# Kernel optimization log

Hardware: AMD Instinct MI355X
Metric: run time of the kernel (lower is better)

## Reference

```python
import jax, jax.numpy as jnp
import numpy as np

M = 4096      # dictionary_size
D = 64        # feature dim
YD = 4        # output dim (y_dim)
FF = 0.999    # forgetting_factor
REG = 1e-2    # regularisation
JITTER = 1e-10
LS = 8.0      # RBF lengthscale


def rbf(a, b):
    # squared-distance RBF Gram via the ||a||^2 + ||b||^2 - 2ab^T identity
    a2 = jnp.sum(a * a, -1)[:, None]
    b2 = jnp.sum(b * b, -1)[None, :]
    d2 = jnp.maximum(a2 + b2 - 2.0 * (a @ b.T), 0.0)
    return jnp.exp(-d2 / (2.0 * LS * LS))


def setup_inputs() -> dict:
    key = jax.random.key(0)
    ks = jax.random.split(key, 7)
    return {
        'dictionary': jax.random.normal(ks[0], (M, D), jnp.float32),
        'mu': jax.random.normal(ks[1], (YD, M, 1), jnp.float32),
        'sigma': jax.random.normal(ks[2], (M, M), jnp.float32),
        'Q': jax.random.normal(ks[3], (M, M), jnp.float32),
        'x': jax.random.normal(ks[4], (D,), jnp.float32),
        'y': jax.random.normal(ks[5], (YD,), jnp.float32),
        'noise_num': jax.random.uniform(ks[6], (YD, 1, 1), jnp.float32),
        'noise_den': jnp.ones((1,), jnp.float32),
        'time_index': jnp.arange(M, dtype=jnp.float32),
        't': M,
    }


def reference(dictionary, mu, sigma, Q, x, y, noise_num, noise_den, time_index, t):
    alloc = time_index >= 0.0                      # (M,) bool: allocated slots
    y_ = y[:, None, None]                          # (YD,1,1)

    # --- B2P forgetting ---
    Kdd = rbf(dictionary, dictionary) * (alloc[:, None] * alloc[None, :])
    sig = FF * sigma + (1.0 - FF) * Kdd
    mu_f = jnp.sqrt(FF) * mu

    # --- kernel evals for new sample ---
    K_dx = rbf(dictionary, x[None, :]) * alloc[:, None]   # (M,1)
    K_xx = rbf(x[None, :], x[None, :]) + JITTER           # (1,1)

    q_ = Q @ K_dx                                         # (M,1)
    pu = jnp.maximum(K_xx - K_dx.T @ q_, 0.0)             # projection uncertainty (1,1)
    h_ = sig @ q_                                         # (M,1)
    npv = jnp.maximum(pu + q_.T @ h_, 0.0)                # noiseless predictive var (1,1)
    pred_mean = q_.T @ mu_f                               # (YD,1,1) via batched matmul
    pv = REG + npv

    # --- augmented (M+1) state ---
    p_ = jnp.concatenate((h_, npv), axis=-2)              # (M+1,1)
    mu_a = jnp.concatenate((mu_f, pred_mean), axis=-2) + (y_ - pred_mean) / pv * p_
    sig_a = jnp.block([[sig, h_], [h_.T, npv]]) - (p_ @ p_.T) / pv
    p2 = jnp.concatenate((q_, -jnp.ones((1, 1), q_.dtype)), axis=0)
    Q_a = jnp.pad(Q, ((0, 1), (0, 1))) + (p2 @ p2.T) / pu

    nnum = noise_num + FF * (y_ - pred_mean) ** 2 / pv
    nden = noise_den + FF

    # --- pruning criterion ---
    x_alloc = jnp.concatenate((alloc, jnp.ones((1,), bool)))

    def crit_low(_):
        return jnp.concatenate((jnp.ones((M, 1), Q_a.dtype), jnp.zeros((1, 1), Q_a.dtype)))

    def crit_mse(_):
        dq = jnp.where(~x_alloc, jnp.inf, jnp.diag(Q_a))
        errors = Q_a @ mu_a / dq[:, None]                 # (YD,M+1,1)
        return jnp.abs(errors).sum(-3)                    # (M+1,1)

    criterion = jax.lax.cond(pu.squeeze() < JITTER, crit_low, crit_mse, None)
    prune = jnp.argmin(criterion)
    denom = jnp.where(~x_alloc[prune], jnp.inf, Q_a[prune, prune])

    # swap (prune <-> last) permutation, then drop last row/col
    perm = jnp.arange(M + 1)
    perm = jnp.where(perm == prune, M, jnp.where(perm == M, prune, perm))

    Q_r = Q_a[perm, :]                                    # row swap
    Qs = Q_r[:-1, prune]                                  # column `prune` after row swap
    Q_n = Q_r[:, perm][:M, :M] - jnp.outer(Qs, Qs) / denom

    mu_n = mu_a[:, perm, :][:, :M, :]
    sig_n = sig_a[perm, :][:, perm][:M, :M]

    dict_n = dictionary.at[prune].set(x)
    ti_n = time_index.at[prune].set(jnp.asarray(t, time_index.dtype))
    alloc_n = ti_n >= 0.0
    sig_n = (alloc_n[:, None] * alloc_n[None, :]) * sig_n
    mu_n = jnp.where((ti_n < 0.0)[:, None], 0.0, mu_n)

    return (mu_n, sig_n, Q_n, dict_n, ti_n, nnum, nden)
```

## Files before the change

kernel.cpp:

```cpp
#include <hip/hip_runtime.h>
#include <math.h>

#define Mn 4096
#define Dn 64

#define OFF_A2   0
#define OFF_K    4096
#define OFF_Q    8192
#define OFF_H    12288
#define OFF_CRIT 20480
#define OFF_QS   32800
#define OFF_QSD  36896
#define SC_PU    40992
#define SC_INVPU 40993
#define SC_NPV   40994
#define SC_PV    40995
#define SC_INVPV 40996
#define SC_DENOM 40997
#define SC_PRUNE 40998
#define SC_DL    41000
#define SC_VY    41004
#define SC_MUAM  41008
#define OFF_DICTB 49152

#define O_MU   0
#define O_SIG  16384
#define O_Q    16793600
#define O_DICT 33570816
#define O_TI   33832960
#define O_NNUM 33837056
#define O_NDEN 33837060

typedef __attribute__((ext_vector_type(8))) __bf16 bf16x8;
typedef __attribute__((ext_vector_type(4))) float f32x4;

__device__ __forceinline__ float waveReduceSum(float v) {
#pragma unroll
    for (int o = 32; o > 0; o >>= 1) v += __shfl_down(v, o);
    return v;
}

__device__ __forceinline__ unsigned short f2bf_rne(float f) {
    unsigned u = __float_as_uint(f);
    unsigned r = (u + 0x7FFFu + ((u >> 16) & 1u)) >> 16;
    return (unsigned short)r;
}

__global__ void k1_prep(const float* __restrict__ dict, const float* __restrict__ x,
                        const float* __restrict__ ti, float* __restrict__ ws) {
    int row  = blockIdx.x * 4 + (threadIdx.x >> 6);
    int lane = threadIdx.x & 63;
    float d  = dict[row * Dn + lane];
    float xv = x[lane];
    ((unsigned short*)(ws + OFF_DICTB))[row * Dn + lane] = f2bf_rne(d);
    float a2 = waveReduceSum(d * d);
    float x2 = waveReduceSum(xv * xv);
    float dx = waveReduceSum(d * xv);
    if (lane == 0) {
        ws[OFF_A2 + row] = a2;
        float d2 = fmaxf(a2 + x2 - 2.0f * dx, 0.0f);
        float kv = expf(d2 * (-1.0f / 128.0f));
        ws[OFF_K + row] = (ti[row] >= 0.0f) ? kv : 0.0f;
    }
}

__global__ void k2_q(const float* __restrict__ Q, float* __restrict__ ws) {
    __shared__ float red[4];
    const int row = blockIdx.x;
    const int tid = threadIdx.x;
    const float4* Qr = (const float4*)(Q + (size_t)row * Mn);
    const float4* kv = (const float4*)(ws + OFF_K);
    float s = 0.0f;
#pragma unroll
    for (int it = 0; it < 4; ++it) {
        int u = tid + it * 256;
        float4 a = Qr[u], b = kv[u];
        s += a.x * b.x + a.y * b.y + a.z * b.z + a.w * b.w;
    }
    s = waveReduceSum(s);
    if ((tid & 63) == 0) red[tid >> 6] = s;
    __syncthreads();
    if (tid == 0) {
        ws[OFF_Q + row] = red[0] + red[1] + red[2] + red[3];
        ws[OFF_H + row] = 0.0f;
    }
}

__global__ __launch_bounds__(256) void k3_h(
        const float* __restrict__ sigma, const float* __restrict__ ti,
        float* __restrict__ ws) {
    const int tid  = threadIdx.x;
    const int lane = tid & 63;
    const int w    = tid >> 6;

    if (blockIdx.x < 1024) {
        const int row = blockIdx.x * 4 + w;
        const float4* S  = (const float4*)(sigma + (size_t)row * Mn);
        const float4* q4 = (const float4*)(ws + OFF_Q);
        float s = 0.0f;
#pragma unroll
        for (int it = 0; it < 16; ++it) {
            int u = lane + it * 64;
            float4 a = S[u], b = q4[u];
            s += a.x * b.x + a.y * b.y + a.z * b.z + a.w * b.w;
        }
        s = waveReduceSum(s);
        if (lane == 0) atomicAdd(ws + OFF_H + row, 0.999f * s);
        return;
    }

    const int t  = blockIdx.x - 1024;
    const int i0 = (t >> 5) * 128 + (w >> 1) * 64;
    const int j0 = (t & 31) * 128 + (w & 1) * 64;
    const int lr = lane >> 4;
    const int lc = lane & 15;
    const uint4* db = (const uint4*)(ws + OFF_DICTB);

    bf16x8 bfrag[4][2];
    float a2j[4], qmj[4];
#pragma unroll
    for (int jt = 0; jt < 4; ++jt) {
        const int col = j0 + jt * 16 + lc;
        bfrag[jt][0] = __builtin_bit_cast(bf16x8, db[col * 8 + lr]);
        bfrag[jt][1] = __builtin_bit_cast(bf16x8, db[col * 8 + 4 + lr]);
        a2j[jt] = ws[OFF_A2 + col];
        float alj = (ti[col] >= 0.0f) ? 1.0f : 0.0f;
        qmj[jt] = 0.001f * alj * ws[OFF_Q + col];
    }

#pragma unroll
    for (int it = 0; it < 4; ++it) {
        const int arow = i0 + it * 16 + lc;
        bf16x8 af0 = __builtin_bit_cast(bf16x8, db[arow * 8 + lr]);
        bf16x8 af1 = __builtin_bit_cast(bf16x8, db[arow * 8 + 4 + lr]);
        float hacc[4] = {0.f, 0.f, 0.f, 0.f};
        float a2i[4], ali[4];
#pragma unroll
        for (int i = 0; i < 4; ++i) {
            const int rg = i0 + it * 16 + lr * 4 + i;
            a2i[i] = ws[OFF_A2 + rg];
            ali[i] = (ti[rg] >= 0.0f) ? 1.0f : 0.0f;
        }
#pragma unroll
        for (int jt = 0; jt < 4; ++jt) {
            f32x4 acc = {0.0f, 0.0f, 0.0f, 0.0f};
            acc = __builtin_amdgcn_mfma_f32_16x16x32_bf16(af0, bfrag[jt][0], acc, 0, 0, 0);
            acc = __builtin_amdgcn_mfma_f32_16x16x32_bf16(af1, bfrag[jt][1], acc, 0, 0, 0);
#pragma unroll
            for (int i = 0; i < 4; ++i) {
                float d2 = fmaxf(a2i[i] + a2j[jt] - 2.0f * acc[i], 0.0f);
                float kv = __expf(d2 * (-1.0f / 128.0f)) * ali[i];
                hacc[i] = fmaf(kv, qmj[jt], hacc[i]);
            }
        }
#pragma unroll
        for (int i = 0; i < 4; ++i) {
            float v = hacc[i];
            v += __shfl_xor(v, 1);
            v += __shfl_xor(v, 2);
            v += __shfl_xor(v, 4);
            v += __shfl_xor(v, 8);
            if (lc == i) atomicAdd(ws + OFF_H + i0 + it * 16 + lr * 4 + i, v);
        }
    }
}

__device__ __forceinline__ float blockReduce1024(float v, float* sred) {
    v = waveReduceSum(v);
    int tid = threadIdx.x;
    __syncthreads();
    if ((tid & 63) == 0) sred[tid >> 6] = v;
    __syncthreads();
    float r = 0.0f;
    if (tid == 0) {
#pragma unroll
        for (int i = 0; i < 16; ++i) r += sred[i];
    }
    return r;
}

__global__ __launch_bounds__(1024) void k4_scalars(
        const float* __restrict__ mu, const float* __restrict__ y,
        const float* __restrict__ nn, const float* __restrict__ nd,
        float* __restrict__ ws, float* __restrict__ out) {
    __shared__ float sred[16];
    const int tid = threadIdx.x;
    const float* k = ws + OFF_K;
    const float* q = ws + OFF_Q;
    const float* h = ws + OFF_H;
    float kq = 0, qh = 0, p0 = 0, p1 = 0, p2 = 0, p3 = 0;
    for (int i = tid; i < Mn; i += 1024) {
        float qi = q[i];
        kq += k[i] * qi;
        qh += qi * h[i];
        p0 += qi * mu[0 * Mn + i];
        p1 += qi * mu[1 * Mn + i];
        p2 += qi * mu[2 * Mn + i];
        p3 += qi * mu[3 * Mn + i];
    }
    float rkq = blockReduce1024(kq, sred);
    float rqh = blockReduce1024(qh, sred);
    float r0 = blockReduce1024(p0, sred);
    float r1 = blockReduce1024(p1, sred);
    float r2 = blockReduce1024(p2, sred);
    float r3 = blockReduce1024(p3, sred);
    if (tid == 0) {
        const float sf = sqrtf(0.999f);
        float pu  = fmaxf(1.0f - rkq, 0.0f);
        float npv = fmaxf(pu + rqh, 0.0f);
        float pv  = 0.01f + npv;
        ws[SC_PU] = pu;
        ws[SC_INVPU] = 1.0f / pu;
        ws[SC_NPV] = npv;
        ws[SC_PV] = pv;
        ws[SC_INVPV] = 1.0f / pv;
        float rr[4] = {r0, r1, r2, r3};
        float critM = 0.0f;
#pragma unroll
        for (int yd = 0; yd < 4; ++yd) {
            float pm = sf * rr[yd];
            float dy = y[yd] - pm;
            float dl = dy / pv;
            float muaM = pm + dl * npv;
            float vy   = (sf * rr[yd] + dl * rqh) - muaM;
            ws[SC_DL + yd]   = dl;
            ws[SC_VY + yd]   = vy;
            ws[SC_MUAM + yd] = muaM;
            critM += fabsf(vy);
            out[O_NNUM + yd] = nn[yd] + 0.999f * (dy * dy) / pv;
        }
        out[O_NDEN] = nd[0] + 0.999f;
        ws[OFF_CRIT + Mn] = (pu < 1e-10f) ? 0.0f : critM;
    }
}

__global__ __launch_bounds__(256) void k5_crit(const float* __restrict__ Q,
                                               const float* __restrict__ mu,
                                               const float* __restrict__ ti,
                                               float* __restrict__ ws) {
    const int row  = blockIdx.x * 4 + (threadIdx.x >> 6);
    const int lane = threadIdx.x & 63;
    const float pu = ws[SC_PU];
    if (pu < 1e-10f) {
        if (lane == 0) ws[OFF_CRIT + row] = 1.0f;
        return;
    }
    const float4* Qr4 = (const float4*)(Q + (size_t)row * Mn);
    const float4* m04 = (const float4*)(mu + 0 * Mn);
    const float4* m14 = (const float4*)(mu + 1 * Mn);
    const float4* m24 = (const float4*)(mu + 2 * Mn);
    const float4* m34 = (const float4*)(mu + 3 * Mn);
    const float4* h4  = (const float4*)(ws + OFF_H);
    float am0 = 0, am1 = 0, am2 = 0, am3 = 0, ah = 0;
#pragma unroll
    for (int it = 0; it < 16; ++it) {
        int u = lane + it * 64;
        float4 qv = Qr4[u];
        float4 a0 = m04[u], a1 = m14[u], a2 = m24[u], a3 = m34[u], hh = h4[u];
        am0 += qv.x * a0.x + qv.y * a0.y + qv.z * a0.z + qv.w * a0.w;
        am1 += qv.x * a1.x + qv.y * a1.y + qv.z * a1.z + qv.w * a1.w;
        am2 += qv.x * a2.x + qv.y * a2.y + qv.z * a2.z + qv.w * a2.w;
        am3 += qv.x * a3.x + qv.y * a3.y + qv.z * a3.z + qv.w * a3.w;
        ah  += qv.x * hh.x + qv.y * hh.y + qv.z * hh.z + qv.w * hh.w;
    }
    am0 = waveReduceSum(am0);
    am1 = waveReduceSum(am1);
    am2 = waveReduceSum(am2);
    am3 = waveReduceSum(am3);
    ah  = waveReduceSum(ah);
    if (lane == 0) {
        const float inv_pu = ws[SC_INVPU];
        const float sf = sqrtf(0.999f);
        float qrow = ws[OFF_Q + row];
        float dq = Q[(size_t)row * Mn + row] + qrow * qrow * inv_pu;
        float crit = 0.0f;
        float am[4] = {am0, am1, am2, am3};
#pragma unroll
        for (int yd = 0; yd < 4; ++yd) {
            float e = sf * am[yd] + ws[SC_DL + yd] * ah + ws[SC_VY + yd] * inv_pu * qrow;
            crit += fabsf(e / dq);
        }
        bool xa = (ti[row] >= 0.0f);
        ws[OFF_CRIT + row] = xa ? crit : 0.0f;
    }
}

__global__ __launch_bounds__(1024) void k6_argmin(const float* __restrict__ Q,
                                                  const float* __restrict__ ti,
                                                  float* __restrict__ ws) {
    __shared__ float sval[1024];
    __shared__ int   sidx[1024];
    const int tid = threadIdx.x;
    float bv = INFINITY;
    int bi = Mn + 1;
    for (int i = tid; i <= Mn; i += 1024) {
        float v = ws[OFF_CRIT + i];
        if (v < bv) { bv = v; bi = i; }
    }
    sval[tid] = bv; sidx[tid] = bi;
    __syncthreads();
    for (int s = 512; s > 0; s >>= 1) {
        if (tid < s) {
            float ov = sval[tid + s]; int oi = sidx[tid + s];
            if (ov < sval[tid] || (ov == sval[tid] && oi < sidx[tid])) {
                sval[tid] = ov; sidx[tid] = oi;
            }
        }
        __syncthreads();
    }
    if (tid == 0) {
        int prune = sidx[0];
        ((int*)ws)[SC_PRUNE] = prune;
        float inv_pu = ws[SC_INVPU];
        bool xa = (prune == Mn) ? true : (ti[prune] >= 0.0f);
        float qap;
        if (prune < Mn) {
            float qp = ws[OFF_Q + prune];
            qap = Q[(size_t)prune * Mn + prune] + qp * qp * inv_pu;
        } else {
            qap = inv_pu;
        }
        ws[SC_DENOM] = xa ? qap : INFINITY;
    }
}

__global__ void k6b_vec(const float* __restrict__ Q, const float* __restrict__ dict,
                        const float* __restrict__ x, const float* __restrict__ ti,
                        const int* __restrict__ tptr, float* __restrict__ ws,
                        float* __restrict__ out) {
    const int tid = blockIdx.x * 256 + threadIdx.x;
    const int prune = ((const int*)ws)[SC_PRUNE];
    const int row = tid >> 6, col = tid & 63;
    out[O_DICT + tid] = (row == prune) ? x[col] : dict[tid];
    if (tid < Mn) {
        float tv = ti[tid];
        if (tid == prune) {
            int raw = *tptr;
            tv = (raw >= 0 && raw < (1 << 30)) ? (float)raw : __int_as_float(raw);
        }
        out[O_TI + tid] = tv;
        const float inv_pu = ws[SC_INVPU];
        const float denom  = ws[SC_DENOM];
        const float p2p = (prune < Mn) ? ws[OFF_Q + prune] : -1.0f;
        float qs;
        if (tid == prune) {
            qs = -p2p * inv_pu;
        } else {
            float base = (prune < Mn) ? Q[(size_t)tid * Mn + prune] : 0.0f;
            qs = base + ws[OFF_Q + tid] * p2p * inv_pu;
        }
        ws[OFF_QS + tid] = qs;
        ws[OFF_QSD + tid] = qs / denom;
    }
}

__global__ __launch_bounds__(256) void k7_fused(const float* __restrict__ Q,
                                                const float* __restrict__ sigma,
                                                const float* __restrict__ mu,
                                                const float* __restrict__ ti,
                                                float* __restrict__ out,
                                                const float* __restrict__ ws) {
    const int tid = threadIdx.x;
    const int prune = ((const int*)ws)[SC_PRUNE];
    const float inv_pu = ws[SC_INVPU];
    const float inv_pv = ws[SC_INVPV];
    const float npv = ws[SC_NPV];

    if (blockIdx.x >= 1024) {
        const int i = blockIdx.x - 1024;
        const int pi = (i == prune) ? Mn : i;
        const bool piok = (pi < Mn);
        const float p2i = piok ? ws[OFF_Q + pi] : -1.0f;
        const float qsi = ws[OFF_QS + i];
        const float4* Qr4  = (const float4*)(Q + (size_t)pi * Mn);
        const float4* q4   = (const float4*)(ws + OFF_Q);
        const float4* qsd4 = (const float4*)(ws + OFF_QSD);
        float4* o4 = (float4*)(out + O_Q + (size_t)i * Mn);
#pragma unroll
        for (int it = 0; it < 4; ++it) {
            int u = tid + it * 256;
            float4 base = piok ? Qr4[u] : make_float4(0.f, 0.f, 0.f, 0.f);
            float4 p2j = q4[u];
            if ((prune >> 2) == u) {
                int c = prune & 3;
                ((float*)&p2j)[c] = -1.0f;
                ((float*)&base)[c] = 0.0f;
            }
            float4 d = qsd4[u];
            float4 r;
            r.x = base.x + p2i * p2j.x * inv_pu - qsi * d.x;
            r.y = base.y + p2i * p2j.y * inv_pu - qsi * d.y;
            r.z = base.z + p2i * p2j.z * inv_pu - qsi * d.z;
            r.w = base.w + p2i * p2j.w * inv_pu - qsi * d.w;
            o4[u] = r;
        }
        if (tid < 4) {
            float tin = out[O_TI + i];
            float v;
            if (tin < 0.0f) v = 0.0f;
            else if (i == prune) v = ws[SC_MUAM + tid];
            else {
                const float sf = sqrtf(0.999f);
                v = sf * mu[tid * Mn + i] + ws[SC_DL + tid] * ws[OFF_H + i];
            }
            out[O_MU + tid * Mn + i] = v;
        }
        return;
    }

    const int t    = blockIdx.x;
    const int lane = tid & 63;
    const int w    = tid >> 6;
    const int i0 = (t >> 5) * 128 + (w >> 1) * 64;
    const int j0 = (t & 31) * 128 + (w & 1) * 64;
    const int lr = lane >> 4;
    const int lc = lane & 15;
    const uint4* db = (const uint4*)(ws + OFF_DICTB);

    bf16x8 bfI[4][2];
    float a2i_s[4], alio_s[4], ain_s[4], hr_s[4];
    bool prow_s[4];
#pragma unroll
    for (int it = 0; it < 4; ++it) {
        const int ri = i0 + it * 16 + lc;
        bfI[it][0] = __builtin_bit_cast(bf16x8, db[ri * 8 + lr]);
        bfI[it][1] = __builtin_bit_cast(bf16x8, db[ri * 8 + 4 + lr]);
        a2i_s[it]  = ws[OFF_A2 + ri];
        alio_s[it] = (ti[ri] >= 0.0f) ? 1.0f : 0.0f;
        ain_s[it]  = (out[O_TI + ri] >= 0.0f) ? 1.0f : 0.0f;
        hr_s[it]   = ws[OFF_H + ri];
        prow_s[it] = (ri == prune);
    }

#pragma unroll
    for (int jt = 0; jt < 4; ++jt) {
        const int jrow = j0 + jt * 16 + lc;
        bf16x8 afJ0 = __builtin_bit_cast(bf16x8, db[jrow * 8 + lr]);
        bf16x8 afJ1 = __builtin_bit_cast(bf16x8, db[jrow * 8 + 4 + lr]);
        const int cb = j0 + jt * 16 + lr * 4;
        const float4 a2j4 = *(const float4*)(ws + OFF_A2 + cb);
        const float4 hj4  = *(const float4*)(ws + OFF_H + cb);
        const float4 tio4 = *(const float4*)(ti + cb);
        const float4 tin4 = *(const float4*)(out + O_TI + cb);
        float a2j[4] = {a2j4.x, a2j4.y, a2j4.z, a2j4.w};
        float hj[4]  = {hj4.x, hj4.y, hj4.z, hj4.w};
        float aljo[4] = {tio4.x >= 0.f ? 1.f : 0.f, tio4.y >= 0.f ? 1.f : 0.f,
                         tio4.z >= 0.f ? 1.f : 0.f, tio4.w >= 0.f ? 1.f : 0.f};
        float ajn[4]  = {tin4.x >= 0.f ? 1.f : 0.f, tin4.y >= 0.f ? 1.f : 0.f,
                         tin4.z >= 0.f ? 1.f : 0.f, tin4.w >= 0.f ? 1.f : 0.f};
        bool pcol[4] = {cb + 0 == prune, cb + 1 == prune, cb + 2 == prune, cb + 3 == prune};
#pragma unroll
        for (int it = 0; it < 4; ++it) {
            f32x4 acc = {0.0f, 0.0f, 0.0f, 0.0f};
            acc = __builtin_amdgcn_mfma_f32_16x16x32_bf16(afJ0, bfI[it][0], acc, 0, 0, 0);
            acc = __builtin_amdgcn_mfma_f32_16x16x32_bf16(afJ1, bfI[it][1], acc, 0, 0, 0);
            const int rg = i0 + it * 16 + lc;
            const size_t off = (size_t)rg * Mn + cb;
            const float4 sv4 = *(const float4*)(sigma + off);
            float sv[4] = {sv4.x, sv4.y, sv4.z, sv4.w};
            float res[4];
#pragma unroll
            for (int e = 0; e < 4; ++e) {
                float d2 = fmaxf(a2i_s[it] + a2j[e] - 2.0f * acc[e], 0.0f);
                float kv = __expf(d2 * (-1.0f / 128.0f)) * alio_s[it] * aljo[e];
                float bs = 0.999f * sv[e] + 0.001f * kv;
                if (pcol[e])    bs = prow_s[it] ? npv : hr_s[it];
                if (prow_s[it]) bs = pcol[e] ? npv : hj[e];
                float p_i = prow_s[it] ? npv : hr_s[it];
                float p_j = pcol[e] ? npv : hj[e];
                res[e] = ain_s[it] * ajn[e] * (bs - p_i * p_j * inv_pv);
            }
            float4 r4 = {res[0], res[1], res[2], res[3]};
            *(float4*)(out + O_SIG + off) = r4;
        }
    }
}

extern "C" void kernel_launch(void* const* d_in, const int* in_sizes, int n_in,
                              void* d_out, int out_size, void* d_ws, size_t ws_size,
                              hipStream_t stream) {
    const float* dict  = (const float*)d_in[0];
    const float* mu    = (const float*)d_in[1];
    const float* sigma = (const float*)d_in[2];
    const float* Q     = (const float*)d_in[3];
    const float* x     = (const float*)d_in[4];
    const float* y     = (const float*)d_in[5];
    const float* nn    = (const float*)d_in[6];
    const float* nd    = (const float*)d_in[7];
    const float* ti    = (const float*)d_in[8];
    const int*   tptr  = (const int*)d_in[9];
    float* out = (float*)d_out;
    float* ws  = (float*)d_ws;

    k1_prep<<<1024, 256, 0, stream>>>(dict, x, ti, ws);
    k2_q<<<4096, 256, 0, stream>>>(Q, ws);
    k3_h<<<2048, 256, 0, stream>>>(sigma, ti, ws);
    k4_scalars<<<1, 1024, 0, stream>>>(mu, y, nn, nd, ws, out);
    k5_crit<<<1024, 256, 0, stream>>>(Q, mu, ti, ws);
    k6_argmin<<<1, 1024, 0, stream>>>(Q, ti, ws);
    k6b_vec<<<1024, 256, 0, stream>>>(Q, dict, x, ti, tptr, ws, out);
    k7_fused<<<5120, 256, 0, stream>>>(Q, sigma, mu, ti, out, ws);
}
```

Baseline: 337.1 us.

## Batch loads ahead of use, prefetch sigma tiles, and use nontemporal stores

Restructures the streaming dot-product kernels so that all global loads for a chunk are issued before the arithmetic, exposing more memory-level parallelism. The fused output kernel now software-prefetches the next sigma tile while computing the current one, and writes Q and sigma outputs with nontemporal stores to avoid polluting cache. It also adds an occupancy hint to the launch bounds. This raises register pressure, which could limit occupancy or cause spills.

```diff
diff --git a/kernel.cpp b/kernel.cpp
--- a/kernel.cpp
+++ b/kernel.cpp
@@ -46,6 +46,11 @@
     return (unsigned short)r;
 }
 
+__device__ __forceinline__ void nt_store4(float* p, float a, float b, float c, float d) {
+    f32x4 v = {a, b, c, d};
+    __builtin_nontemporal_store(v, (f32x4*)p);
+}
+
 __global__ void k1_prep(const float* __restrict__ dict, const float* __restrict__ x,
                         const float* __restrict__ ti, float* __restrict__ ws) {
     int row  = blockIdx.x * 4 + (threadIdx.x >> 6);
@@ -64,19 +69,22 @@
     }
 }
 
-__global__ void k2_q(const float* __restrict__ Q, float* __restrict__ ws) {
+__global__ __launch_bounds__(256, 4) void k2_q(const float* __restrict__ Q,
+                                               float* __restrict__ ws) {
     __shared__ float red[4];
     const int row = blockIdx.x;
     const int tid = threadIdx.x;
     const float4* Qr = (const float4*)(Q + (size_t)row * Mn);
     const float4* kv = (const float4*)(ws + OFF_K);
+    float4 a[4], b[4];
+#pragma unroll
+    for (int it = 0; it < 4; ++it) a[it] = Qr[tid + it * 256];
+#pragma unroll
+    for (int it = 0; it < 4; ++it) b[it] = kv[tid + it * 256];
     float s = 0.0f;
 #pragma unroll
-    for (int it = 0; it < 4; ++it) {
-        int u = tid + it * 256;
-        float4 a = Qr[u], b = kv[u];
-        s += a.x * b.x + a.y * b.y + a.z * b.z + a.w * b.w;
-    }
+    for (int it = 0; it < 4; ++it)
+        s += a[it].x * b[it].x + a[it].y * b[it].y + a[it].z * b[it].z + a[it].w * b[it].w;
     s = waveReduceSum(s);
     if ((tid & 63) == 0) red[tid >> 6] = s;
     __syncthreads();
@@ -86,7 +94,7 @@
     }
 }
 
-__global__ __launch_bounds__(256) void k3_h(
+__global__ __launch_bounds__(256, 4) void k3_h(
         const float* __restrict__ sigma, const float* __restrict__ ti,
         float* __restrict__ ws) {
     const int tid  = threadIdx.x;
@@ -99,10 +107,15 @@
         const float4* q4 = (const float4*)(ws + OFF_Q);
         float s = 0.0f;
 #pragma unroll
-        for (int it = 0; it < 16; ++it) {
-            int u = lane + it * 64;
-            float4 a = S[u], b = q4[u];
-            s += a.x * b.x + a.y * b.y + a.z * b.z + a.w * b.w;
+        for (int c = 0; c < 2; ++c) {
+            float4 a[8], b[8];
+#pragma unroll
+            for (int j = 0; j < 8; ++j) a[j] = S[lane + (c * 8 + j) * 64];
+#pragma unroll
+            for (int j = 0; j < 8; ++j) b[j] = q4[lane + (c * 8 + j) * 64];
+#pragma unroll
+            for (int j = 0; j < 8; ++j)
+                s += a[j].x * b[j].x + a[j].y * b[j].y + a[j].z * b[j].z + a[j].w * b[j].w;
         }
         s = waveReduceSum(s);
         if (lane == 0) atomicAdd(ws + OFF_H + row, 0.999f * s);
@@ -234,10 +247,10 @@
     }
 }
 
-__global__ __launch_bounds__(256) void k5_crit(const float* __restrict__ Q,
-                                               const float* __restrict__ mu,
-                                               const float* __restrict__ ti,
-                                               float* __restrict__ ws) {
+__global__ __launch_bounds__(256, 4) void k5_crit(const float* __restrict__ Q,
+                                                  const float* __restrict__ mu,
+                                                  const float* __restrict__ ti,
+                                                  float* __restrict__ ws) {
     const int row  = blockIdx.x * 4 + (threadIdx.x >> 6);
     const int lane = threadIdx.x & 63;
     const float pu = ws[SC_PU];
@@ -253,15 +266,20 @@
     const float4* h4  = (const float4*)(ws + OFF_H);
     float am0 = 0, am1 = 0, am2 = 0, am3 = 0, ah = 0;
 #pragma unroll
-    for (int it = 0; it < 16; ++it) {
-        int u = lane + it * 64;
-        float4 qv = Qr4[u];
-        float4 a0 = m04[u], a1 = m14[u], a2 = m24[u], a3 = m34[u], hh = h4[u];
-        am0 += qv.x * a0.x + qv.y * a0.y + qv.z * a0.z + qv.w * a0.w;
-        am1 += qv.x * a1.x + qv.y * a1.y + qv.z * a1.z + qv.w * a1.w;
-        am2 += qv.x * a2.x + qv.y * a2.y + qv.z * a2.z + qv.w * a2.w;
-        am3 += qv.x * a3.x + qv.y * a3.y + qv.z * a3.z + qv.w * a3.w;
-        ah  += qv.x * hh.x + qv.y * hh.y + qv.z * hh.z + qv.w * hh.w;
+    for (int c = 0; c < 4; ++c) {
+        float4 qv[4];
+#pragma unroll
+        for (int j = 0; j < 4; ++j) qv[j] = Qr4[lane + (c * 4 + j) * 64];
+#pragma unroll
+        for (int j = 0; j < 4; ++j) {
+            int u = lane + (c * 4 + j) * 64;
+            float4 a0 = m04[u], a1 = m14[u], a2 = m24[u], a3 = m34[u], hh = h4[u];
+            am0 += qv[j].x * a0.x + qv[j].y * a0.y + qv[j].z * a0.z + qv[j].w * a0.w;
+            am1 += qv[j].x * a1.x + qv[j].y * a1.y + qv[j].z * a1.z + qv[j].w * a1.w;
+            am2 += qv[j].x * a2.x + qv[j].y * a2.y + qv[j].z * a2.z + qv[j].w * a2.w;
+            am3 += qv[j].x * a3.x + qv[j].y * a3.y + qv[j].z * a3.z + qv[j].w * a3.w;
+            ah  += qv[j].x * hh.x + qv[j].y * hh.y + qv[j].z * hh.z + qv[j].w * hh.w;
+        }
     }
     am0 = waveReduceSum(am0);
     am1 = waveReduceSum(am1);
@@ -354,12 +372,12 @@
     }
 }
 
-__global__ __launch_bounds__(256) void k7_fused(const float* __restrict__ Q,
-                                                const float* __restrict__ sigma,
-                                                const float* __restrict__ mu,
-                                                const float* __restrict__ ti,
-                                                float* __restrict__ out,
-                                                const float* __restrict__ ws) {
+__global__ __launch_bounds__(256, 4) void k7_fused(const float* __restrict__ Q,
+                                                   const float* __restrict__ sigma,
+                                                   const float* __restrict__ mu,
+                                                   const float* __restrict__ ti,
+                                                   float* __restrict__ out,
+                                                   const float* __restrict__ ws) {
     const int tid = threadIdx.x;
     const int prune = ((const int*)ws)[SC_PRUNE];
     const float inv_pu = ws[SC_INVPU];
@@ -375,24 +393,30 @@
         const float4* Qr4  = (const float4*)(Q + (size_t)pi * Mn);
         const float4* q4   = (const float4*)(ws + OFF_Q);
         const float4* qsd4 = (const float4*)(ws + OFF_QSD);
-        float4* o4 = (float4*)(out + O_Q + (size_t)i * Mn);
+        float* orow = out + O_Q + (size_t)i * Mn;
+        float4 base[4], p2j[4], d[4];
 #pragma unroll
         for (int it = 0; it < 4; ++it) {
             int u = tid + it * 256;
-            float4 base = piok ? Qr4[u] : make_float4(0.f, 0.f, 0.f, 0.f);
-            float4 p2j = q4[u];
+            base[it] = piok ? Qr4[u] : make_float4(0.f, 0.f, 0.f, 0.f);
+        }
+#pragma unroll
+        for (int it = 0; it < 4; ++it) p2j[it] = q4[tid + it * 256];
+#pragma unroll
+        for (int it = 0; it < 4; ++it) d[it] = qsd4[tid + it * 256];
+#pragma unroll
+        for (int it = 0; it < 4; ++it) {
+            int u = tid + it * 256;
             if ((prune >> 2) == u) {
                 int c = prune & 3;
-                ((float*)&p2j)[c] = -1.0f;
-                ((float*)&base)[c] = 0.0f;
+                ((float*)&p2j[it])[c] = -1.0f;
+                ((float*)&base[it])[c] = 0.0f;
             }
-            float4 d = qsd4[u];
-            float4 r;
-            r.x = base.x + p2i * p2j.x * inv_pu - qsi * d.x;
-            r.y = base.y + p2i * p2j.y * inv_pu - qsi * d.y;
-            r.z = base.z + p2i * p2j.z * inv_pu - qsi * d.z;
-            r.w = base.w + p2i * p2j.w * inv_pu - qsi * d.w;
-            o4[u] = r;
+            nt_store4(orow + u * 4,
+                      base[it].x + p2i * p2j[it].x * inv_pu - qsi * d[it].x,
+                      base[it].y + p2i * p2j[it].y * inv_pu - qsi * d[it].y,
+                      base[it].z + p2i * p2j[it].z * inv_pu - qsi * d[it].z,
+                      base[it].w + p2i * p2j[it].w * inv_pu - qsi * d[it].w);
         }
         if (tid < 4) {
             float tin = out[O_TI + i];
@@ -432,8 +456,22 @@
         prow_s[it] = (ri == prune);
     }
 
+    const float* sigbase = sigma + (size_t)(i0 + lc) * Mn + j0 + lr * 4;
+    float* outbase = out + O_SIG + (size_t)(i0 + lc) * Mn + j0 + lr * 4;
+
+    float4 sv[4];
+#pragma unroll
+    for (int it = 0; it < 4; ++it)
+        sv[it] = *(const float4*)(sigbase + (size_t)it * 16 * Mn);
+
 #pragma unroll
     for (int jt = 0; jt < 4; ++jt) {
+        float4 svn[4];
+        if (jt < 3) {
+#pragma unroll
+            for (int it = 0; it < 4; ++it)
+                svn[it] = *(const float4*)(sigbase + (size_t)it * 16 * Mn + (jt + 1) * 16);
+        }
         const int jrow = j0 + jt * 16 + lc;
         bf16x8 afJ0 = __builtin_bit_cast(bf16x8, db[jrow * 8 + lr]);
         bf16x8 afJ1 = __builtin_bit_cast(bf16x8, db[jrow * 8 + 4 + lr]);
@@ -454,25 +492,24 @@
             f32x4 acc = {0.0f, 0.0f, 0.0f, 0.0f};
             acc = __builtin_amdgcn_mfma_f32_16x16x32_bf16(afJ0, bfI[it][0], acc, 0, 0, 0);
             acc = __builtin_amdgcn_mfma_f32_16x16x32_bf16(afJ1, bfI[it][1], acc, 0, 0, 0);
-            const int rg = i0 + it * 16 + lc;
-            const size_t off = (size_t)rg * Mn + cb;
-            const float4 sv4 = *(const float4*)(sigma + off);
-            float sv[4] = {sv4.x, sv4.y, sv4.z, sv4.w};
+            float sve[4] = {sv[it].x, sv[it].y, sv[it].z, sv[it].w};
             float res[4];
 #pragma unroll
             for (int e = 0; e < 4; ++e) {
                 float d2 = fmaxf(a2i_s[it] + a2j[e] - 2.0f * acc[e], 0.0f);
                 float kv = __expf(d2 * (-1.0f / 128.0f)) * alio_s[it] * aljo[e];
-                float bs = 0.999f * sv[e] + 0.001f * kv;
+                float bs = 0.999f * sve[e] + 0.001f * kv;
                 if (pcol[e])    bs = prow_s[it] ? npv : hr_s[it];
                 if (prow_s[it]) bs = pcol[e] ? npv : hj[e];
                 float p_i = prow_s[it] ? npv : hr_s[it];
                 float p_j = pcol[e] ? npv : hj[e];
                 res[e] = ain_s[it] * ajn[e] * (bs - p_i * p_j * inv_pv);
             }
-            float4 r4 = {res[0], res[1], res[2], res[3]};
-            *(float4*)(out + O_SIG + off) = r4;
-        }
+            nt_store4(outbase + (size_t)it * 16 * Mn + jt * 16,
+                      res[0], res[1], res[2], res[3]);
+        }
+#pragma unroll
+        for (int it = 0; it < 4; ++it) sv[it] = svn[it];
     }
 }
 
```

Result: slower. 369.5 us (+9.6%).

## Fold scalar and argmin single-block kernels into redundant per-block prologues; prefetch sigma

Applied to the files above, without the earlier changes.

The single-block scalar-reduction kernel is merged into the criterion kernel: every block redundantly recomputes the six dot products over 4096 elements, and block 0 writes the shared scalars. Likewise the argmin over the criterion vector is recomputed by every block of the vector kernel. This removes two serialized one-block launches and their dependency bubbles, at the price of redundant global reads of q, k, h, mu and the criterion array in each of the 1024 blocks. The fused sigma-update kernel also software-prefetches the next sigma tile into registers to overlap loads with MFMA/exp work, which raises register pressure.

```diff
diff --git a/kernel.cpp b/kernel.cpp
--- a/kernel.cpp
+++ b/kernel.cpp
@@ -165,55 +165,52 @@
     }
 }
 
-__device__ __forceinline__ float blockReduce1024(float v, float* sred) {
-    v = waveReduceSum(v);
-    int tid = threadIdx.x;
-    __syncthreads();
-    if ((tid & 63) == 0) sred[tid >> 6] = v;
-    __syncthreads();
-    float r = 0.0f;
-    if (tid == 0) {
-#pragma unroll
-        for (int i = 0; i < 16; ++i) r += sred[i];
-    }
-    return r;
-}
-
-__global__ __launch_bounds__(1024) void k4_scalars(
-        const float* __restrict__ mu, const float* __restrict__ y,
-        const float* __restrict__ nn, const float* __restrict__ nd,
-        float* __restrict__ ws, float* __restrict__ out) {
-    __shared__ float sred[16];
-    const int tid = threadIdx.x;
-    const float* k = ws + OFF_K;
-    const float* q = ws + OFF_Q;
-    const float* h = ws + OFF_H;
+__global__ __launch_bounds__(256) void k5_crit(const float* __restrict__ Q,
+                                               const float* __restrict__ mu,
+                                               const float* __restrict__ ti,
+                                               const float* __restrict__ y,
+                                               const float* __restrict__ nn,
+                                               const float* __restrict__ nd,
+                                               float* __restrict__ ws,
+                                               float* __restrict__ out) {
+    __shared__ float wred[4][6];
+    __shared__ float sc[12];
+    const int tid  = threadIdx.x;
+    const int lane = tid & 63;
+    const int wv   = tid >> 6;
+    const float* kk = ws + OFF_K;
+    const float* q  = ws + OFF_Q;
+    const float* h  = ws + OFF_H;
+
     float kq = 0, qh = 0, p0 = 0, p1 = 0, p2 = 0, p3 = 0;
-    for (int i = tid; i < Mn; i += 1024) {
+    for (int i = tid; i < Mn; i += 256) {
         float qi = q[i];
-        kq += k[i] * qi;
+        kq += kk[i] * qi;
         qh += qi * h[i];
         p0 += qi * mu[0 * Mn + i];
         p1 += qi * mu[1 * Mn + i];
         p2 += qi * mu[2 * Mn + i];
         p3 += qi * mu[3 * Mn + i];
     }
-    float rkq = blockReduce1024(kq, sred);
-    float rqh = blockReduce1024(qh, sred);
-    float r0 = blockReduce1024(p0, sred);
-    float r1 = blockReduce1024(p1, sred);
-    float r2 = blockReduce1024(p2, sred);
-    float r3 = blockReduce1024(p3, sred);
+    kq = waveReduceSum(kq); qh = waveReduceSum(qh);
+    p0 = waveReduceSum(p0); p1 = waveReduceSum(p1);
+    p2 = waveReduceSum(p2); p3 = waveReduceSum(p3);
+    if (lane == 0) {
+        wred[wv][0] = kq; wred[wv][1] = qh; wred[wv][2] = p0;
+        wred[wv][3] = p1; wred[wv][4] = p2; wred[wv][5] = p3;
+    }
+    __syncthreads();
     if (tid == 0) {
+        float rkq = 0, rqh = 0, r0 = 0, r1 = 0, r2 = 0, r3 = 0;
+#pragma unroll
+        for (int wj = 0; wj < 4; ++wj) {
+            rkq += wred[wj][0]; rqh += wred[wj][1]; r0 += wred[wj][2];
+            r1  += wred[wj][3]; r2  += wred[wj][4]; r3 += wred[wj][5];
+        }
         const float sf = sqrtf(0.999f);
         float pu  = fmaxf(1.0f - rkq, 0.0f);
         float npv = fmaxf(pu + rqh, 0.0f);
         float pv  = 0.01f + npv;
-        ws[SC_PU] = pu;
-        ws[SC_INVPU] = 1.0f / pu;
-        ws[SC_NPV] = npv;
-        ws[SC_PV] = pv;
-        ws[SC_INVPV] = 1.0f / pv;
         float rr[4] = {r0, r1, r2, r3};
         float critM = 0.0f;
 #pragma unroll
@@ -223,24 +220,27 @@
             float dl = dy / pv;
             float muaM = pm + dl * npv;
             float vy   = (sf * rr[yd] + dl * rqh) - muaM;
-            ws[SC_DL + yd]   = dl;
-            ws[SC_VY + yd]   = vy;
-            ws[SC_MUAM + yd] = muaM;
+            sc[yd] = dl;
+            sc[4 + yd] = vy;
             critM += fabsf(vy);
-            out[O_NNUM + yd] = nn[yd] + 0.999f * (dy * dy) / pv;
-        }
-        out[O_NDEN] = nd[0] + 0.999f;
-        ws[OFF_CRIT + Mn] = (pu < 1e-10f) ? 0.0f : critM;
-    }
-}
-
-__global__ __launch_bounds__(256) void k5_crit(const float* __restrict__ Q,
-                                               const float* __restrict__ mu,
-                                               const float* __restrict__ ti,
-                                               float* __restrict__ ws) {
-    const int row  = blockIdx.x * 4 + (threadIdx.x >> 6);
-    const int lane = threadIdx.x & 63;
-    const float pu = ws[SC_PU];
+            if (blockIdx.x == 0) {
+                ws[SC_DL + yd] = dl; ws[SC_VY + yd] = vy; ws[SC_MUAM + yd] = muaM;
+                out[O_NNUM + yd] = nn[yd] + 0.999f * (dy * dy) / pv;
+            }
+        }
+        sc[8] = pu;
+        sc[9] = 1.0f / pu;
+        if (blockIdx.x == 0) {
+            ws[SC_PU] = pu; ws[SC_INVPU] = 1.0f / pu; ws[SC_NPV] = npv;
+            ws[SC_PV] = pv; ws[SC_INVPV] = 1.0f / pv;
+            out[O_NDEN] = nd[0] + 0.999f;
+            ws[OFF_CRIT + Mn] = (pu < 1e-10f) ? 0.0f : critM;
+        }
+    }
+    __syncthreads();
+
+    const float pu = sc[8];
+    const int row = blockIdx.x * 4 + wv;
     if (pu < 1e-10f) {
         if (lane == 0) ws[OFF_CRIT + row] = 1.0f;
         return;
@@ -269,7 +269,7 @@
     am3 = waveReduceSum(am3);
     ah  = waveReduceSum(ah);
     if (lane == 0) {
-        const float inv_pu = ws[SC_INVPU];
+        const float inv_pu = sc[9];
         const float sf = sqrtf(0.999f);
         float qrow = ws[OFF_Q + row];
         float dq = Q[(size_t)row * Mn + row] + qrow * qrow * inv_pu;
@@ -277,7 +277,7 @@
         float am[4] = {am0, am1, am2, am3};
 #pragma unroll
         for (int yd = 0; yd < 4; ++yd) {
-            float e = sf * am[yd] + ws[SC_DL + yd] * ah + ws[SC_VY + yd] * inv_pu * qrow;
+            float e = sf * am[yd] + sc[yd] * ah + sc[4 + yd] * inv_pu * qrow;
             crit += fabsf(e / dq);
         }
         bool xa = (ti[row] >= 0.0f);
@@ -285,32 +285,37 @@
     }
 }
 
-__global__ __launch_bounds__(1024) void k6_argmin(const float* __restrict__ Q,
-                                                  const float* __restrict__ ti,
-                                                  float* __restrict__ ws) {
-    __shared__ float sval[1024];
-    __shared__ int   sidx[1024];
-    const int tid = threadIdx.x;
+__global__ __launch_bounds__(256) void k6b_vec(const float* __restrict__ Q,
+                                               const float* __restrict__ dict,
+                                               const float* __restrict__ x,
+                                               const float* __restrict__ ti,
+                                               const int* __restrict__ tptr,
+                                               float* __restrict__ ws,
+                                               float* __restrict__ out) {
+    __shared__ float sval[256];
+    __shared__ int   sidx[256];
+    __shared__ float sden[1];
+    __shared__ int   sprune[1];
+    const int t = threadIdx.x;
     float bv = INFINITY;
     int bi = Mn + 1;
-    for (int i = tid; i <= Mn; i += 1024) {
+    for (int i = t; i <= Mn; i += 256) {
         float v = ws[OFF_CRIT + i];
         if (v < bv) { bv = v; bi = i; }
     }
-    sval[tid] = bv; sidx[tid] = bi;
+    sval[t] = bv; sidx[t] = bi;
     __syncthreads();
-    for (int s = 512; s > 0; s >>= 1) {
-        if (tid < s) {
-            float ov = sval[tid + s]; int oi = sidx[tid + s];
-            if (ov < sval[tid] || (ov == sval[tid] && oi < sidx[tid])) {
-                sval[tid] = ov; sidx[tid] = oi;
+    for (int s = 128; s > 0; s >>= 1) {
+        if (t < s) {
+            float ov = sval[t + s]; int oi = sidx[t + s];
+            if (ov < sval[t] || (ov == sval[t] && oi < sidx[t])) {
+                sval[t] = ov; sidx[t] = oi;
             }
         }
         __syncthreads();
     }
-    if (tid == 0) {
+    if (t == 0) {
         int prune = sidx[0];
-        ((int*)ws)[SC_PRUNE] = prune;
         float inv_pu = ws[SC_INVPU];
         bool xa = (prune == Mn) ? true : (ti[prune] >= 0.0f);
         float qap;
@@ -320,16 +325,17 @@
         } else {
             qap = inv_pu;
         }
-        ws[SC_DENOM] = xa ? qap : INFINITY;
-    }
-}
-
-__global__ void k6b_vec(const float* __restrict__ Q, const float* __restrict__ dict,
-                        const float* __restrict__ x, const float* __restrict__ ti,
-                        const int* __restrict__ tptr, float* __restrict__ ws,
-                        float* __restrict__ out) {
+        float den = xa ? qap : INFINITY;
+        sprune[0] = prune; sden[0] = den;
+        if (blockIdx.x == 0) {
+            ((int*)ws)[SC_PRUNE] = prune;
+            ws[SC_DENOM] = den;
+        }
+    }
+    __syncthreads();
+    const int prune = sprune[0];
+    const float denom = sden[0];
     const int tid = blockIdx.x * 256 + threadIdx.x;
-    const int prune = ((const int*)ws)[SC_PRUNE];
     const int row = tid >> 6, col = tid & 63;
     out[O_DICT + tid] = (row == prune) ? x[col] : dict[tid];
     if (tid < Mn) {
@@ -340,7 +346,6 @@
         }
         out[O_TI + tid] = tv;
         const float inv_pu = ws[SC_INVPU];
-        const float denom  = ws[SC_DENOM];
         const float p2p = (prune < Mn) ? ws[OFF_Q + prune] : -1.0f;
         float qs;
         if (tid == prune) {
@@ -381,17 +386,21 @@
             int u = tid + it * 256;
             float4 base = piok ? Qr4[u] : make_float4(0.f, 0.f, 0.f, 0.f);
             float4 p2j = q4[u];
-            if ((prune >> 2) == u) {
-                int c = prune & 3;
-                ((float*)&p2j)[c] = -1.0f;
-                ((float*)&base)[c] = 0.0f;
-            }
             float4 d = qsd4[u];
+            const int j4 = u * 4;
+            const bool q0 = (j4 + 0) == prune;
+            const bool q1 = (j4 + 1) == prune;
+            const bool q2 = (j4 + 2) == prune;
+            const bool q3 = (j4 + 3) == prune;
+            float px = q0 ? -1.0f : p2j.x;  float bx = q0 ? 0.0f : base.x;
+            float py = q1 ? -1.0f : p2j.y;  float by = q1 ? 0.0f : base.y;
+            float pz = q2 ? -1.0f : p2j.z;  float bz = q2 ? 0.0f : base.z;
+            float pw = q3 ? -1.0f : p2j.w;  float bw = q3 ? 0.0f : base.w;
             float4 r;
-            r.x = base.x + p2i * p2j.x * inv_pu - qsi * d.x;
-            r.y = base.y + p2i * p2j.y * inv_pu - qsi * d.y;
-            r.z = base.z + p2i * p2j.z * inv_pu - qsi * d.z;
-            r.w = base.w + p2i * p2j.w * inv_pu - qsi * d.w;
+            r.x = bx + p2i * px * inv_pu - qsi * d.x;
+            r.y = by + p2i * py * inv_pu - qsi * d.y;
+            r.z = bz + p2i * pz * inv_pu - qsi * d.z;
+            r.w = bw + p2i * pw * inv_pu - qsi * d.w;
             o4[u] = r;
         }
         if (tid < 4) {
@@ -432,8 +441,22 @@
         prow_s[it] = (ri == prune);
     }
 
+    const float* sigbase = sigma + (size_t)(i0 + lc) * Mn + j0 + lr * 4;
+    float* outbase = out + O_SIG + (size_t)(i0 + lc) * Mn + j0 + lr * 4;
+
+    float4 sv[4];
+#pragma unroll
+    for (int it = 0; it < 4; ++it)
+        sv[it] = *(const float4*)(sigbase + (size_t)it * 16 * Mn);
+
 #pragma unroll
     for (int jt = 0; jt < 4; ++jt) {
+        float4 svn[4];
+        if (jt < 3) {
+#pragma unroll
+            for (int it = 0; it < 4; ++it)
+                svn[it] = *(const float4*)(sigbase + (size_t)it * 16 * Mn + (jt + 1) * 16);
+        }
         const int jrow = j0 + jt * 16 + lc;
         bf16x8 afJ0 = __builtin_bit_cast(bf16x8, db[jrow * 8 + lr]);
         bf16x8 afJ1 = __builtin_bit_cast(bf16x8, db[jrow * 8 + 4 + lr]);
@@ -454,16 +477,13 @@
             f32x4 acc = {0.0f, 0.0f, 0.0f, 0.0f};
             acc = __builtin_amdgcn_mfma_f32_16x16x32_bf16(afJ0, bfI[it][0], acc, 0, 0, 0);
             acc = __builtin_amdgcn_mfma_f32_16x16x32_bf16(afJ1, bfI[it][1], acc, 0, 0, 0);
-            const int rg = i0 + it * 16 + lc;
-            const size_t off = (size_t)rg * Mn + cb;
-            const float4 sv4 = *(const float4*)(sigma + off);
-            float sv[4] = {sv4.x, sv4.y, sv4.z, sv4.w};
+            float sve[4] = {sv[it].x, sv[it].y, sv[it].z, sv[it].w};
             float res[4];
 #pragma unroll
             for (int e = 0; e < 4; ++e) {
                 float d2 = fmaxf(a2i_s[it] + a2j[e] - 2.0f * acc[e], 0.0f);
                 float kv = __expf(d2 * (-1.0f / 128.0f)) * alio_s[it] * aljo[e];
-                float bs = 0.999f * sv[e] + 0.001f * kv;
+                float bs = 0.999f * sve[e] + 0.001f * kv;
                 if (pcol[e])    bs = prow_s[it] ? npv : hr_s[it];
                 if (prow_s[it]) bs = pcol[e] ? npv : hj[e];
                 float p_i = prow_s[it] ? npv : hr_s[it];
@@ -471,8 +491,10 @@
                 res[e] = ain_s[it] * ajn[e] * (bs - p_i * p_j * inv_pv);
             }
             float4 r4 = {res[0], res[1], res[2], res[3]};
-            *(float4*)(out + O_SIG + off) = r4;
-        }
+            *(float4*)(outbase + (size_t)it * 16 * Mn + jt * 16) = r4;
+        }
+#pragma unroll
+        for (int it = 0; it < 4; ++it) sv[it] = svn[it];
     }
 }
 
@@ -495,9 +517,7 @@
     k1_prep<<<1024, 256, 0, stream>>>(dict, x, ti, ws);
     k2_q<<<4096, 256, 0, stream>>>(Q, ws);
     k3_h<<<2048, 256, 0, stream>>>(sigma, ti, ws);
-    k4_scalars<<<1, 1024, 0, stream>>>(mu, y, nn, nd, ws, out);
-    k5_crit<<<1024, 256, 0, stream>>>(Q, mu, ti, ws);
-    k6_argmin<<<1, 1024, 0, stream>>>(Q, ti, ws);
+    k5_crit<<<1024, 256, 0, stream>>>(Q, mu, ti, y, nn, nd, ws, out);
     k6b_vec<<<1024, 256, 0, stream>>>(Q, dict, x, ti, tptr, ws, out);
     k7_fused<<<5120, 256, 0, stream>>>(Q, sigma, mu, ti, out, ws);
 }
```

Result: no change. 339.2 us (+0.6%).
